# Kernel optimization log

Measured on AMD Instinct MI355X. Metric: run time of the kernel, lower is better.

The kernel has to match this reference:

```python
import jax, jax.numpy as jnp
import numpy as np

B, H, W = 2, 224, 224
E, NH, DH, DFF = 64, 4, 16, 2048


def _conv2d(x, w, b):
    # stride-1 3x3 conv, padding=1 == SAME
    y = jax.lax.conv_general_dilated(x, w, (1, 1), 'SAME',
                                     dimension_numbers=('NCHW', 'OIHW', 'NCHW'))
    return y + b[None, :, None, None]


def _layer_norm(x, g, b, eps=1e-5):
    mu = x.mean(-1, keepdims=True)
    xc = x - mu
    var = (xc * xc).mean(-1, keepdims=True)
    return g * xc * jax.lax.rsqrt(var + eps) + b


def setup_inputs() -> dict:
    key = jax.random.key(0)
    ks = jax.random.split(key, 16)
    rn = lambda k, shape, s=0.05: jax.random.normal(k, shape, dtype=jnp.float32) * s
    z = lambda n: jnp.zeros((n,), jnp.float32)
    return {
        'x': jax.random.normal(ks[0], (B, 3, H, W), dtype=jnp.float32),
        'enc_w1': rn(ks[1], (64, 3, 3, 3)), 'enc_b1': z(64),
        'enc_w2': rn(ks[2], (64, 64, 3, 3)), 'enc_b2': z(64),
        'in_proj_w': rn(ks[3], (3 * E, E)), 'in_proj_b': z(3 * E),
        'out_proj_w': rn(ks[4], (E, E)), 'out_proj_b': z(E),
        'ln1_g': jnp.ones((E,), jnp.float32), 'ln1_b': z(E),
        'ffn_w1': rn(ks[5], (DFF, E)), 'ffn_b1': z(DFF),
        'ffn_w2': rn(ks[6], (E, DFF)), 'ffn_b2': z(E),
        'ln2_g': jnp.ones((E,), jnp.float32), 'ln2_b': z(E),
        'sf_w1': rn(ks[7], (32, 64, 3, 3)), 'sf_b1': z(32),
        'sf_w2': rn(ks[8], (9, 32, 3, 3)), 'sf_b2': z(9),
        'dec_w1': rn(ks[9], (64, 1, 3, 3)), 'dec_b1': z(64),
        'dec_w2': rn(ks[10], (1, 64, 3, 3)), 'dec_b2': z(1),
    }


def _forward(x, enc_w1, enc_b1, enc_w2, enc_b2,
             in_proj_w, in_proj_b, out_proj_w, out_proj_b,
             ln1_g, ln1_b, ffn_w1, ffn_b1, ffn_w2, ffn_b2, ln2_g, ln2_b,
             sf_w1, sf_b1, sf_w2, sf_b2, dec_w1, dec_b1, dec_w2, dec_b2):
    # ---- encoder ----
    e = jax.nn.relu(_conv2d(x, enc_w1, enc_b1))
    e = jax.nn.relu(_conv2d(e, enc_w2, enc_b2))
    b, c, h, w = e.shape
    # torch TransformerEncoderLayer default batch_first=False: [B, HW, E] is (S=B, N=HW, E)
    t = e.reshape(b, c, h * w).transpose(0, 2, 1)  # [S=B, N=HW, E]
    qkv = t @ in_proj_w.T + in_proj_b
    q, k, v = jnp.split(qkv, 3, axis=-1)
    S, N = q.shape[0], q.shape[1]
    q = q.reshape(S, N, NH, DH)
    k = k.reshape(S, N, NH, DH)
    v = v.reshape(S, N, NH, DH)
    scores = jnp.einsum('snhd,tnhd->nhst', q, k) / np.float32(np.sqrt(DH))
    attn = jnp.einsum('nhst,tnhd->snhd', jax.nn.softmax(scores, axis=-1), v)
    attn = attn.reshape(S, N, E) @ out_proj_w.T + out_proj_b
    t = _layer_norm(t + attn, ln1_g, ln1_b)
    ff = jax.nn.relu(t @ ffn_w1.T + ffn_b1) @ ffn_w2.T + ffn_b2
    t = _layer_norm(t + ff, ln2_g, ln2_b)
    enc2 = t.transpose(0, 2, 1).reshape(b, c, h, w)
    # ---- spatially adaptive per-pixel 3x3 filter (KPN-style) ----
    f = _conv2d(_conv2d(enc2, sf_w1, sf_b1), sf_w2, sf_b2)
    filters = f.reshape(b, 3, 3, h, w)  # per-pixel 3x3 kernel
    s = x.sum(axis=1)  # accumulate over the 3 input channels -> [B,H,W]
    sp = jnp.pad(s, ((0, 0), (1, 1), (1, 1)))
    patches = jnp.stack([sp[:, u:u + h, v:v + w] for u in range(3) for v in range(3)],
                        axis=1).reshape(b, 3, 3, h, w)
    fused = (filters * patches).sum(axis=(1, 2))[:, None]  # [B,1,H,W]
    # ---- decoder ----
    d = jax.nn.relu(_conv2d(fused, dec_w1, dec_b1))
    return jax.nn.sigmoid(_conv2d(d, dec_w2, dec_b2))


def reference(x, enc_w1, enc_b1, enc_w2, enc_b2,
              in_proj_w, in_proj_b, out_proj_w, out_proj_b,
              ln1_g, ln1_b, ffn_w1, ffn_b1, ffn_w2, ffn_b2, ln2_g, ln2_b,
              sf_w1, sf_b1, sf_w2, sf_b2, dec_w1, dec_b1, dec_w2, dec_b2):
    return _forward(x, enc_w1, enc_b1, enc_w2, enc_b2,
                    in_proj_w, in_proj_b, out_proj_w, out_proj_b,
                    ln1_g, ln1_b, ffn_w1, ffn_b1, ffn_w2, ffn_b2, ln2_g, ln2_b,
                    sf_w1, sf_b1, sf_w2, sf_b2, dec_w1, dec_b1, dec_w2, dec_b2)
```

## Files before the change

kernel.cpp:

```cpp
#include <hip/hip_runtime.h>
#include <hip/hip_bf16.h>
#include <cstddef>

#define HW   50176
#define NPIX 100352
#define IW   224

typedef unsigned short ushort_t;
typedef __attribute__((ext_vector_type(8))) short bf16x8;
typedef __attribute__((ext_vector_type(8))) unsigned short ushort8;
typedef __attribute__((ext_vector_type(4))) float f32x4;
typedef __attribute__((ext_vector_type(2))) _Float16 f16x2;
typedef __attribute__((ext_vector_type(8))) _Float16 f16x8;

__device__ inline ushort_t f2bf(float f) {
    __hip_bfloat16 h = __float2bfloat16(f);
    return __builtin_bit_cast(ushort_t, h);
}
__device__ inline float bf2f(ushort_t u) {
    return __uint_as_float(((unsigned)u) << 16);
}
__device__ inline bf16x8 ldg8(const ushort_t* p) {
    return *reinterpret_cast<const bf16x8*>(p);
}
__device__ inline void b2f8(const ushort_t* p, float* f) {
    ushort8 v = *reinterpret_cast<const ushort8*>(p);
#pragma unroll
    for (int i = 0; i < 8; i++) f[i] = bf2f(v[i]);
}
__device__ inline f16x2 pk16(float a, float b) {
    return __builtin_bit_cast(f16x2, __builtin_amdgcn_cvt_pkrtz(a, b));
}

__device__ inline void dma16(const ushort_t* g, ushort_t* l) {
    __builtin_amdgcn_global_load_lds(
        (const __attribute__((address_space(1))) void*)g,
        (__attribute__((address_space(3))) void*)l, 16, 0, 0);
}

__device__ void conv1_body(int gid, const float* __restrict__ x,
                           const float* __restrict__ w,
                           const float* __restrict__ bias,
                           ushort_t* __restrict__ out)
{
    int b = gid >= HW;
    int p = gid - b * HW;
    int y = p / IW, xx = p - y * IW;

    float v[27];
#pragma unroll
    for (int ci = 0; ci < 3; ci++) {
        const float* ip = x + ((size_t)(b * 3 + ci)) * HW;
#pragma unroll
        for (int t = 0; t < 9; t++) {
            int dy = t / 3 - 1, dx = t % 3 - 1;
            int yy = y + dy, xc = xx + dx;
            float tv = 0.f;
            if ((unsigned)yy < (unsigned)IW && (unsigned)xc < (unsigned)IW)
                tv = ip[yy * IW + xc];
            v[ci * 9 + t] = tv;
        }
    }
#pragma unroll
    for (int g = 0; g < 8; g++) {
        ushort8 o8;
#pragma unroll
        for (int i = 0; i < 8; i++) {
            int co = g * 8 + i;
            float a = bias[co];
            const float* wp = w + co * 27;
#pragma unroll
            for (int k = 0; k < 27; k++) a = fmaf(v[k], wp[k], a);
            o8[i] = f2bf(fmaxf(a, 0.f));
        }
        *reinterpret_cast<ushort8*>(out + (size_t)gid * 64 + g * 8) = o8;
    }
}

__global__ __launch_bounds__(256) void prep_conv1_k(
    const float* __restrict__ x,     const float* __restrict__ enc_w1,
    const float* __restrict__ enc_b1, ushort_t* __restrict__ E1b,
    const float* __restrict__ in_w,  ushort_t* __restrict__ in_wb,
    const float* __restrict__ out_w, ushort_t* __restrict__ out_wb,
    const float* __restrict__ w1,    ushort_t* __restrict__ w1p,
    const float* __restrict__ w2,    _Float16* __restrict__ w2s,
    const float* __restrict__ ec2,   ushort_t* __restrict__ wc2p,
    const float* __restrict__ s1,    ushort_t* __restrict__ ws1p,
    const float* __restrict__ s2,    ushort_t* __restrict__ ws2)
{
    if (blockIdx.x < 392) {
        conv1_body(blockIdx.x * 256 + threadIdx.x, x, enc_w1, enc_b1, E1b);
        return;
    }
    int idx = (blockIdx.x - 392) * 256 + threadIdx.x;
    if (idx < 12288) { in_wb[idx] = f2bf(in_w[idx]); return; }
    idx -= 12288;
    if (idx < 4096)  { out_wb[idx] = f2bf(out_w[idx]); return; }
    idx -= 4096;
    if (idx < 131072){
        int j = idx >> 6, e = idx & 63;
        int c = j >> 6, jl = j & 63;
        w1p[(size_t)c * 6144 + jl * 72 + e] = f2bf(w1[idx]);
        return;
    }
    idx -= 131072;
    if (idx < 131072){
        int j    = idx & 7;
        int lane = (idx >> 3) & 63;
        int rest = idx >> 9;
        int nt   = rest & 3;
        int cp   = rest >> 2;
        int p    = cp & 1;
        int c    = cp >> 1;
        int quad = lane >> 4;
        int e2   = nt * 16 + (lane & 15);
        int hl   = (j < 4) ? (quad * 4 + j) : (16 + quad * 4 + (j - 4));
        int hidden = c * 64 + p * 32 + hl;
        w2s[idx] = (_Float16)w2[(size_t)e2 * 2048 + hidden];
        return;
    }
    idx -= 131072;
    if (idx < 36864) {
        int j    = idx & 7;
        int lane = (idx >> 3) & 63;
        int rest = idx >> 9;
        int ks   = rest & 1;
        int nt   = (rest >> 1) & 3;
        int t    = rest >> 3;
        int co   = nt * 16 + (lane & 15);
        int ci   = ks * 32 + (lane >> 4) * 8 + j;
        wc2p[idx] = f2bf(ec2[((size_t)co * 64 + ci) * 9 + t]);
        return;
    }
    idx -= 36864;
    if (idx < 18432) {
        int j    = idx & 7;
        int lane = (idx >> 3) & 63;
        int rest = idx >> 9;
        int ks   = rest & 1;
        int nt   = (rest >> 1) & 1;
        int t    = rest >> 2;
        int co   = nt * 16 + (lane & 15);
        int ci   = ks * 32 + (lane >> 4) * 8 + j;
        ws1p[idx] = f2bf(s1[((size_t)co * 64 + ci) * 9 + t]);
        return;
    }
    idx -= 18432;
    if (idx < 4608)  {
        int ci = idx % 32;
        int t  = (idx / 32) % 9;
        int co = idx / 288;
        ws2[idx] = (co < 9) ? f2bf(s2[((size_t)co * 32 + ci) * 9 + t]) : (ushort_t)0;
        return;
    }
}

__global__ __launch_bounds__(256, 2) void enc2xf_k(
    const ushort_t* __restrict__ E1b, const ushort_t* __restrict__ Wc2p,
    const float* __restrict__ enc_b2,
    const ushort_t* __restrict__ Wqkv, const float* __restrict__ Bqkv,
    const ushort_t* __restrict__ Wo, const float* __restrict__ Bo,
    const float* __restrict__ g, const float* __restrict__ be,
    ushort_t* __restrict__ T1b)
{
    __shared__ ushort_t Q[128 * 200];
    __shared__ ushort_t WT[9216];

    int tid = threadIdx.x, wave = tid >> 6, lane = tid & 63;
    int lm = lane & 15, quad = lane >> 4;
    int p0 = blockIdx.x * 64;

    {
        int lr0 = wave * 32;
        int m[2], py[2], px[2];
#pragma unroll
        for (int mt = 0; mt < 2; mt++) {
            int lr = lr0 + mt * 16 + lm;
            int gp = p0 + (lr & 63);
            m[mt] = (lr >> 6) * HW + gp;
            py[mt] = gp / IW;
            px[mt] = gp - py[mt] * IW;
        }

        f32x4 acc[2][4] = {};
        bf16x8 zz = {};
        bf16x8 af[9][2][2];

#pragma unroll
        for (int t = 0; t < 9; t++) {
            int dy = t / 3 - 1, dx = t % 3 - 1;
#pragma unroll
            for (int mt = 0; mt < 2; mt++) {
                bool ok = (unsigned)(py[mt] + dy) < (unsigned)IW &&
                          (unsigned)(px[mt] + dx) < (unsigned)IW;
                const ushort_t* ip = E1b + (size_t)(m[mt] + dy * IW + dx) * 64 + quad * 8;
#pragma unroll
                for (int ks = 0; ks < 2; ks++)
                    af[t][mt][ks] = ok ? ldg8(ip + ks * 32) : zz;
            }
        }

#pragma unroll
        for (int t = 0; t < 9; t++) {
#pragma unroll
            for (int nt = 0; nt < 4; nt++)
#pragma unroll
                for (int ks = 0; ks < 2; ks++) {
                    bf16x8 bfv = ldg8(Wc2p + (size_t)(t * 8 + nt * 2 + ks) * 512 + lane * 8);
#pragma unroll
                    for (int mt = 0; mt < 2; mt++)
                        acc[mt][nt] = __builtin_amdgcn_mfma_f32_16x16x32_bf16(
                            af[t][mt][ks], bfv, acc[mt][nt], 0, 0, 0);
                }
        }

#pragma unroll
        for (int nt = 0; nt < 4; nt++) {
            float bv = enc_b2[nt * 16 + lm];
#pragma unroll
            for (int mt = 0; mt < 2; mt++)
#pragma unroll
                for (int r = 0; r < 4; r++) {
                    int lr = lr0 + mt * 16 + quad * 4 + r;
                    WT[lr * 72 + nt * 16 + lm] =
                        f2bf(fmaxf(acc[mt][nt][r] + bv, 0.f));
                }
        }
    }

    bf16x8 wq[12][2];
#pragma unroll
    for (int nt = 0; nt < 12; nt++)
#pragma unroll
        for (int ks = 0; ks < 2; ks++)
            wq[nt][ks] = ldg8(Wqkv + (size_t)(nt * 16 + lm) * 64 + ks * 32 + quad * 8);

    __syncthreads();

#pragma unroll
    for (int mt = 0; mt < 2; mt++) {
        int lA = mt * 64 + wave * 16;
        bf16x8 a[2];
#pragma unroll
        for (int ks = 0; ks < 2; ks++)
            a[ks] = *reinterpret_cast<const bf16x8*>(
                &WT[(lA + lm) * 72 + ks * 32 + quad * 8]);
        f32x4 acc[12] = {};
#pragma unroll
        for (int nt = 0; nt < 12; nt++)
#pragma unroll
            for (int ks = 0; ks < 2; ks++)
                acc[nt] = __builtin_amdgcn_mfma_f32_16x16x32_bf16(
                    a[ks], wq[nt][ks], acc[nt], 0, 0, 0);
        int lrow = lA + quad * 4;
#pragma unroll
        for (int nt = 0; nt < 12; nt++) {
            float bb = Bqkv[nt * 16 + lm];
#pragma unroll
            for (int r = 0; r < 4; r++)
                Q[(lrow + r) * 200 + nt * 16 + lm] = f2bf(acc[nt][r] + bb);
        }
    }
    __syncthreads();

    {
        int px = tid >> 2, h = tid & 3;
        ushort_t* r0 = &Q[px * 200 + h * 16];
        ushort_t* r1 = &Q[(64 + px) * 200 + h * 16];

        float q0[16], k0[16], v0[16], q1[16], k1[16], v1[16];
        b2f8(r0,       q0); b2f8(r0 + 8,   q0 + 8);
        b2f8(r0 + 64,  k0); b2f8(r0 + 72,  k0 + 8);
        b2f8(r0 + 128, v0); b2f8(r0 + 136, v0 + 8);
        b2f8(r1,       q1); b2f8(r1 + 8,   q1 + 8);
        b2f8(r1 + 64,  k1); b2f8(r1 + 72,  k1 + 8);
        b2f8(r1 + 128, v1); b2f8(r1 + 136, v1 + 8);

        float s00 = 0, s01 = 0, s10 = 0, s11 = 0;
#pragma unroll
        for (int d = 0; d < 16; d++) {
            s00 += q0[d] * k0[d]; s01 += q0[d] * k1[d];
            s10 += q1[d] * k0[d]; s11 += q1[d] * k1[d];
        }
        s00 *= 0.25f; s01 *= 0.25f; s10 *= 0.25f; s11 *= 0.25f;

        float m0 = fmaxf(s00, s01);
        float e00 = __expf(s00 - m0), e01 = __expf(s01 - m0);
        float i0 = 1.f / (e00 + e01);
        float p00 = e00 * i0, p01 = e01 * i0;

        float m1 = fmaxf(s10, s11);
        float e10 = __expf(s10 - m1), e11 = __expf(s11 - m1);
        float i1 = 1.f / (e10 + e11);
        float p10 = e10 * i1, p11 = e11 * i1;

#pragma unroll
        for (int c = 0; c < 2; c++) {
            ushort8 a0v, a1v;
#pragma unroll
            for (int i = 0; i < 8; i++) {
                int d = c * 8 + i;
                a0v[i] = f2bf(p00 * v0[d] + p01 * v1[d]);
                a1v[i] = f2bf(p10 * v0[d] + p11 * v1[d]);
            }
            *reinterpret_cast<ushort8*>(r0 + c * 8) = a0v;
            *reinterpret_cast<ushort8*>(r1 + c * 8) = a1v;
        }
    }

    bf16x8 wo[4][2];
#pragma unroll
    for (int nt = 0; nt < 4; nt++)
#pragma unroll
        for (int ks = 0; ks < 2; ks++)
            wo[nt][ks] = ldg8(Wo + (size_t)(nt * 16 + lm) * 64 + ks * 32 + quad * 8);

    __syncthreads();

#pragma unroll
    for (int mt = 0; mt < 2; mt++) {
        int lA = mt * 64 + wave * 16;
        size_t gbase = (size_t)((mt == 0 ? p0 : HW + p0) + wave * 16);
        bf16x8 a[2];
#pragma unroll
        for (int ks = 0; ks < 2; ks++)
            a[ks] = *reinterpret_cast<const bf16x8*>(
                &Q[(lA + lm) * 200 + ks * 32 + quad * 8]);
        f32x4 acc[4] = {};
#pragma unroll
        for (int nt = 0; nt < 4; nt++)
#pragma unroll
            for (int ks = 0; ks < 2; ks++)
                acc[nt] = __builtin_amdgcn_mfma_f32_16x16x32_bf16(
                    a[ks], wo[nt][ks], acc[nt], 0, 0, 0);

        float bv[4], gv[4], bev[4];
#pragma unroll
        for (int nt = 0; nt < 4; nt++) {
            bv[nt]  = Bo[nt * 16 + lm];
            gv[nt]  = g[nt * 16 + lm];
            bev[nt] = be[nt * 16 + lm];
        }
#pragma unroll
        for (int r = 0; r < 4; r++) {
            int lr = lA + quad * 4 + r;
            size_t row = gbase + quad * 4 + r;
            float v[4]; float s = 0.f;
#pragma unroll
            for (int nt = 0; nt < 4; nt++) {
                v[nt] = acc[nt][r] + bv[nt] + bf2f(WT[lr * 72 + nt * 16 + lm]);
                s += v[nt];
            }
#pragma unroll
            for (int o = 8; o; o >>= 1) s += __shfl_xor(s, o, 64);
            float mu = s * 0.015625f;
            float q = 0.f;
#pragma unroll
            for (int nt = 0; nt < 4; nt++) { v[nt] -= mu; q += v[nt] * v[nt]; }
#pragma unroll
            for (int o = 8; o; o >>= 1) q += __shfl_xor(q, o, 64);
            float rstd = rsqrtf(q * 0.015625f + 1e-5f);
#pragma unroll
            for (int nt = 0; nt < 4; nt++)
                T1b[row * 64 + nt * 16 + lm] = f2bf(gv[nt] * v[nt] * rstd + bev[nt]);
        }
    }
}

__global__ __launch_bounds__(256, 2) void neconv2_k(
    const ushort_t* __restrict__ In, const ushort_t* __restrict__ Wp,
    const float* __restrict__ bias, ushort_t* __restrict__ Ob)
{
    int tid = threadIdx.x, wave = tid >> 6, lane = tid & 63;
    int lm = lane & 15, quad = lane >> 4;
    int m0 = blockIdx.x * 128 + wave * 32;

    int m[2], py[2], px[2];
#pragma unroll
    for (int mt = 0; mt < 2; mt++) {
        int mm = m0 + mt * 16 + lm;
        m[mt] = mm;
        int p = mm - (mm >= HW ? HW : 0);
        py[mt] = p / IW;
        px[mt] = p - py[mt] * IW;
    }

    f32x4 acc[2][2] = {};
    bf16x8 zz = {};
    bf16x8 af[9][2][2];

#pragma unroll
    for (int t = 0; t < 9; t++) {
        int dy = t / 3 - 1, dx = t % 3 - 1;
#pragma unroll
        for (int mt = 0; mt < 2; mt++) {
            bool ok = (unsigned)(py[mt] + dy) < (unsigned)IW &&
                      (unsigned)(px[mt] + dx) < (unsigned)IW;
            const ushort_t* ip = In + (size_t)(m[mt] + dy * IW + dx) * 64 + quad * 8;
#pragma unroll
            for (int ks = 0; ks < 2; ks++)
                af[t][mt][ks] = ok ? ldg8(ip + ks * 32) : zz;
        }
    }

#pragma unroll
    for (int t = 0; t < 9; t++) {
#pragma unroll
        for (int nt = 0; nt < 2; nt++)
#pragma unroll
            for (int ks = 0; ks < 2; ks++) {
                bf16x8 bfv = ldg8(Wp + (size_t)(t * 4 + nt * 2 + ks) * 512 + lane * 8);
#pragma unroll
                for (int mt = 0; mt < 2; mt++)
                    acc[mt][nt] = __builtin_amdgcn_mfma_f32_16x16x32_bf16(
                        af[t][mt][ks], bfv, acc[mt][nt], 0, 0, 0);
            }
    }

#pragma unroll
    for (int nt = 0; nt < 2; nt++) {
        int col = nt * 16 + lm;
        float bv = bias[col];
#pragma unroll
        for (int mt = 0; mt < 2; mt++)
#pragma unroll
            for (int r = 0; r < 4; r++) {
                int row = m0 + mt * 16 + quad * 4 + r;
                Ob[(size_t)row * 32 + col] = f2bf(acc[mt][nt][r] + bv);
            }
    }
}

__global__ __launch_bounds__(512) void ffn9_k(
    const ushort_t* __restrict__ T1b,
    const ushort_t* __restrict__ W1p, const float* __restrict__ B1,
    const _Float16* __restrict__ W2s, const float* __restrict__ B2,
    const float* __restrict__ g, const float* __restrict__ be,
    ushort_t* __restrict__ OutTb)
{
    __shared__ ushort_t W1lds[3][6144];
    __shared__ ushort_t W2lds[3][4096];
    __shared__ float    B1l[2048];

    int tid = threadIdx.x, wave = tid >> 6, lane = tid & 63;
    int lm = lane & 15, quad = lane >> 4;
    int rowbase = blockIdx.x * 256 + wave * 32;

    *reinterpret_cast<float4*>(&B1l[tid * 4]) =
        *reinterpret_cast<const float4*>(B1 + tid * 4);

    bf16x8 Bt[2][2];
#pragma unroll
    for (int mt = 0; mt < 2; mt++)
#pragma unroll
        for (int ks = 0; ks < 2; ks++)
            Bt[mt][ks] = ldg8(T1b + (size_t)(rowbase + mt * 16 + lm) * 64 + ks * 32 + quad * 8);

    __syncthreads();

    auto dma_chunk = [&](int c, int pb) {
        const ushort_t* g1 = W1p + (size_t)c * 6144;
        const ushort_t* g2 = (const ushort_t*)(W2s + (size_t)c * 4096);
#pragma unroll
        for (int i = 0; i < 3; i++) {
            int idx = i * 8 + wave;
            if (idx < 12)
                dma16(g1 + idx * 512 + lane * 8, &W1lds[pb][idx * 512]);
            else if (idx < 20)
                dma16(g2 + (idx - 12) * 512 + lane * 8,
                      &W2lds[pb][(idx - 12) * 512]);
        }
    };

    dma_chunk(0, 0);
    dma_chunk(1, 1);

    f32x4 acc[2][4] = {};

    for (int c = 0; c < 32; c++) {
        int pb = c % 3;

        if (c < 31) {
            if (wave < 4) asm volatile("s_waitcnt vmcnt(3)" ::: "memory");
            else          asm volatile("s_waitcnt vmcnt(2)" ::: "memory");
        } else {
            asm volatile("s_waitcnt vmcnt(0)" ::: "memory");
        }
        __builtin_amdgcn_s_barrier();
        asm volatile("" ::: "memory");

        if (c + 2 < 32) dma_chunk(c + 2, (c + 2) % 3);

        const ushort_t* w1l = &W1lds[pb][0];
        const ushort_t* w2l = &W2lds[pb][0];

#pragma unroll
        for (int p = 0; p < 2; p++) {
            bf16x8 w1r[2][2];
            f16x8  w2r[4];
            float4 b1r[2];
#pragma unroll
            for (int s = 0; s < 2; s++) {
                int ul = p * 2 + s;
#pragma unroll
                for (int ks = 0; ks < 2; ks++)
                    w1r[s][ks] = *reinterpret_cast<const bf16x8*>(
                        &w1l[(ul * 16 + lm) * 72 + ks * 32 + quad * 8]);
                b1r[s] = *reinterpret_cast<const float4*>(
                    &B1l[(c * 4 + ul) * 16 + quad * 4]);
            }
#pragma unroll
            for (int nt = 0; nt < 4; nt++)
                w2r[nt] = *reinterpret_cast<const f16x8*>(
                    &w2l[((p * 4 + nt) * 64 + lane) * 8]);

            f32x4 h[2][2];
#pragma unroll
            for (int s = 0; s < 2; s++) {
                f32x4 binit = {b1r[s].x, b1r[s].y, b1r[s].z, b1r[s].w};
#pragma unroll
                for (int mt = 0; mt < 2; mt++) h[s][mt] = binit;
            }

            __builtin_amdgcn_s_setprio(1);
#pragma unroll
            for (int s = 0; s < 2; s++)
#pragma unroll
                for (int ks = 0; ks < 2; ks++)
#pragma unroll
                    for (int mt = 0; mt < 2; mt++)
                        h[s][mt] = __builtin_amdgcn_mfma_f32_16x16x32_bf16(
                            w1r[s][ks], Bt[mt][ks], h[s][mt], 0, 0, 0);

            f16x8 aH[2];
#pragma unroll
            for (int mt = 0; mt < 2; mt++) {
                f16x2 t0 = pk16(fmaxf(h[0][mt][0], 0.f), fmaxf(h[0][mt][1], 0.f));
                f16x2 t1 = pk16(fmaxf(h[0][mt][2], 0.f), fmaxf(h[0][mt][3], 0.f));
                f16x2 t2 = pk16(fmaxf(h[1][mt][0], 0.f), fmaxf(h[1][mt][1], 0.f));
                f16x2 t3 = pk16(fmaxf(h[1][mt][2], 0.f), fmaxf(h[1][mt][3], 0.f));
                f16x8 a;
                a[0] = t0[0]; a[1] = t0[1]; a[2] = t1[0]; a[3] = t1[1];
                a[4] = t2[0]; a[5] = t2[1]; a[6] = t3[0]; a[7] = t3[1];
                aH[mt] = a;
            }

#pragma unroll
            for (int nt = 0; nt < 4; nt++)
#pragma unroll
                for (int mt = 0; mt < 2; mt++)
                    acc[mt][nt] = __builtin_amdgcn_mfma_f32_16x16x32_f16(
                        aH[mt], w2r[nt], acc[mt][nt], 0, 0, 0);
            __builtin_amdgcn_s_setprio(0);
        }
    }

    float b2v[4], gv[4], bev[4];
#pragma unroll
    for (int nt = 0; nt < 4; nt++) {
        b2v[nt] = B2[nt * 16 + lm];
        gv[nt]  = g[nt * 16 + lm];
        bev[nt] = be[nt * 16 + lm];
    }
#pragma unroll
    for (int mt = 0; mt < 2; mt++)
#pragma unroll
        for (int r = 0; r < 4; r++) {
            int row = rowbase + mt * 16 + quad * 4 + r;
            float v[4]; float s = 0.f;
#pragma unroll
            for (int nt = 0; nt < 4; nt++) {
                v[nt] = acc[mt][nt][r] + b2v[nt] +
                        bf2f(T1b[(size_t)row * 64 + nt * 16 + lm]);
                s += v[nt];
            }
#pragma unroll
            for (int o = 8; o; o >>= 1) s += __shfl_xor(s, o, 64);
            float mu = s * 0.015625f;
            float q = 0.f;
#pragma unroll
            for (int nt = 0; nt < 4; nt++) { v[nt] -= mu; q += v[nt] * v[nt]; }
#pragma unroll
            for (int o = 8; o; o >>= 1) q += __shfl_xor(q, o, 64);
            float rstd = rsqrtf(q * 0.015625f + 1e-5f);
#pragma unroll
            for (int nt = 0; nt < 4; nt++)
                OutTb[(size_t)row * 64 + nt * 16 + lm] =
                    f2bf(gv[nt] * v[nt] * rstd + bev[nt]);
        }
}

__global__ __launch_bounds__(256) void sf2kpn_k(
    const ushort_t* __restrict__ In,
    const ushort_t* __restrict__ Wsw,
    const float* __restrict__ bias,
    const float* __restrict__ x,
    float* __restrict__ fused)
{
    __shared__ float Fl[128 * 12];
    int tid = threadIdx.x, wave = tid >> 6, lane = tid & 63;
    int lm = lane & 15, quad = lane >> 4;
    int m0 = blockIdx.x * 128 + wave * 32;

    int m[2], py[2], px[2];
#pragma unroll
    for (int mt = 0; mt < 2; mt++) {
        int mm = m0 + mt * 16 + lm;
        m[mt] = mm;
        int p = mm - (mm >= HW ? HW : 0);
        py[mt] = p / IW;
        px[mt] = p - py[mt] * IW;
    }

    f32x4 acc[2] = {};
    bf16x8 zz = {};
    bf16x8 af[9][2];
    bf16x8 wv[9];

#pragma unroll
    for (int t = 0; t < 9; t++) {
        int dy = t / 3 - 1, dx = t % 3 - 1;
#pragma unroll
        for (int mt = 0; mt < 2; mt++) {
            bool ok = (unsigned)(py[mt] + dy) < (unsigned)IW &&
                      (unsigned)(px[mt] + dx) < (unsigned)IW;
            af[t][mt] = ok ? ldg8(In + (size_t)(m[mt] + dy * IW + dx) * 32 + quad * 8) : zz;
        }
    }
#pragma unroll
    for (int t = 0; t < 9; t++)
        wv[t] = ldg8(Wsw + ((size_t)lm * 9 + t) * 32 + quad * 8);

#pragma unroll
    for (int t = 0; t < 9; t++)
#pragma unroll
        for (int mt = 0; mt < 2; mt++)
            acc[mt] = __builtin_amdgcn_mfma_f32_16x16x32_bf16(af[t][mt], wv[t], acc[mt], 0, 0, 0);

    if (lm < 9) {
        float bv = bias[lm];
#pragma unroll
        for (int mt = 0; mt < 2; mt++)
#pragma unroll
            for (int r = 0; r < 4; r++) {
                int lrow = wave * 32 + mt * 16 + quad * 4 + r;
                Fl[lrow * 12 + lm] = acc[mt][r] + bv;
            }
    }
    __syncthreads();

    if (tid < 128) {
        int gid = blockIdx.x * 128 + tid;
        int b = gid >= HW;
        int p = gid - b * HW;
        int y = p / IW, xx = p - y * IW;
        const float* fp = &Fl[tid * 12];
        const float* xp = x + (size_t)b * 3 * HW;
        float a = 0.f;
#pragma unroll
        for (int u = 0; u < 3; u++) {
            int yy = y + u - 1;
            if ((unsigned)yy >= (unsigned)IW) continue;
#pragma unroll
            for (int v = 0; v < 3; v++) {
                int xc = xx + v - 1;
                if ((unsigned)xc >= (unsigned)IW) continue;
                int o = yy * IW + xc;
                float s = xp[o] + xp[HW + o] + xp[2 * HW + o];
                a += fp[u * 3 + v] * s;
            }
        }
        fused[gid] = a;
    }
}

__global__ __launch_bounds__(256) void dec_tile_k(
    const float* __restrict__ fused,
    const float* __restrict__ w1, const float* __restrict__ b1,
    const float* __restrict__ w2, const float* __restrict__ b2,
    float* __restrict__ out)
{
    __shared__ float    Fs[400];
    __shared__ _Float16 Hl[324 * 72];

    int tid = threadIdx.x;
    int b   = blockIdx.x / 196;
    int rem = blockIdx.x - b * 196;
    int ty0 = (rem / 14) * 16;
    int tx0 = (rem % 14) * 16;
    const float* fp = fused + (size_t)b * HW;

    for (int k = tid; k < 400; k += 256) {
        int fy = k / 20, fx = k - fy * 20;
        int gy = ty0 + fy - 2, gx = tx0 + fx - 2;
        float t = 0.f;
        if ((unsigned)gy < (unsigned)IW && (unsigned)gx < (unsigned)IW)
            t = fp[gy * IW + gx];
        Fs[k] = t;
    }
    __syncthreads();

    for (int ph = tid; ph < 324; ph += 256) {
        int hy = ph / 18, hx = ph - hy * 18;
        int gy = ty0 + hy - 1, gx = tx0 + hx - 1;
        _Float16* op = &Hl[ph * 72];
        if ((unsigned)gy >= (unsigned)IW || (unsigned)gx >= (unsigned)IW) {
            f16x8 z = {};
#pragma unroll
            for (int g = 0; g < 8; g++)
                *reinterpret_cast<f16x8*>(op + g * 8) = z;
        } else {
            float F[9];
#pragma unroll
            for (int s = 0; s < 9; s++)
                F[s] = Fs[(hy + s / 3) * 20 + (hx + s % 3)];
#pragma unroll
            for (int g = 0; g < 8; g++) {
                f16x8 o;
#pragma unroll
                for (int i = 0; i < 8; i++) {
                    int c = g * 8 + i;
                    float h = b1[c];
                    const float* wp = w1 + c * 9;
#pragma unroll
                    for (int s = 0; s < 9; s++) h = fmaf(F[s], wp[s], h);
                    o[i] = (_Float16)fmaxf(h, 0.f);
                }
                *reinterpret_cast<f16x8*>(op + g * 8) = o;
            }
        }
    }
    __syncthreads();

    {
        int ty = tid >> 4, tx = tid & 15;
        int gy = ty0 + ty, gx = tx0 + tx;
        float acc = b2[0];
#pragma unroll
        for (int n = 0; n < 9; n++) {
            int dy = n / 3 - 1, dx = n % 3 - 1;
            int yy = gy + dy, xc = gx + dx;
            if ((unsigned)yy >= (unsigned)IW || (unsigned)xc >= (unsigned)IW) continue;
            const _Float16* hp = &Hl[((ty + 1 + dy) * 18 + (tx + 1 + dx)) * 72];
#pragma unroll
            for (int g = 0; g < 8; g++) {
                f16x8 hv = *reinterpret_cast<const f16x8*>(hp + g * 8);
#pragma unroll
                for (int i = 0; i < 8; i++)
                    acc = fmaf((float)hv[i], w2[(g * 8 + i) * 9 + n], acc);
            }
        }
        out[(size_t)b * HW + gy * IW + gx] = 1.f / (1.f + __expf(-acc));
    }
}

extern "C" void kernel_launch(void* const* d_in, const int* in_sizes, int n_in,
                              void* d_out, int out_size, void* d_ws, size_t ws_size,
                              hipStream_t stream)
{
    const float* x      = (const float*)d_in[0];
    const float* enc_w1 = (const float*)d_in[1];
    const float* enc_b1 = (const float*)d_in[2];
    const float* enc_w2 = (const float*)d_in[3];
    const float* enc_b2 = (const float*)d_in[4];
    const float* in_w   = (const float*)d_in[5];
    const float* in_b   = (const float*)d_in[6];
    const float* out_w  = (const float*)d_in[7];
    const float* out_b  = (const float*)d_in[8];
    const float* ln1_g  = (const float*)d_in[9];
    const float* ln1_b  = (const float*)d_in[10];
    const float* ffn_w1 = (const float*)d_in[11];
    const float* ffn_b1 = (const float*)d_in[12];
    const float* ffn_w2 = (const float*)d_in[13];
    const float* ffn_b2 = (const float*)d_in[14];
    const float* ln2_g  = (const float*)d_in[15];
    const float* ln2_b  = (const float*)d_in[16];
    const float* sf_w1  = (const float*)d_in[17];
    const float* sf_b1  = (const float*)d_in[18];
    const float* sf_w2  = (const float*)d_in[19];
    const float* sf_b2  = (const float*)d_in[20];
    const float* dec_w1 = (const float*)d_in[21];
    const float* dec_b1 = (const float*)d_in[22];
    const float* dec_w2 = (const float*)d_in[23];
    const float* dec_b2 = (const float*)d_in[24];

    float* ws = (float*)d_ws;
    const size_t SZ = (size_t)NPIX * 64;

    ushort_t* E1b  = (ushort_t*)(ws + 5 * SZ);
    ushort_t* Tb   = (ushort_t*)(ws + 11 * SZ / 2);
    ushort_t* wu   = (ushort_t*)(ws + 6 * SZ);
    ushort_t* in_wb  = wu;
    ushort_t* out_wb = wu + 12288;
    ushort_t* w1p    = wu + 16384;
    _Float16* w2s    = (_Float16*)(wu + 212992);
    ushort_t* wc2p   = wu + 344064;
    ushort_t* ws1p   = wu + 385536;
    ushort_t* ws2    = wu + 408576;
    float*    base3 = ws + 3 * SZ;
    ushort_t* s1b   = (ushort_t*)base3;
    float*    fused = base3 + SZ / 2;

    prep_conv1_k<<<1714, 256, 0, stream>>>(
        x, enc_w1, enc_b1, E1b,
        in_w, in_wb, out_w, out_wb, ffn_w1, w1p,
        ffn_w2, w2s, enc_w2, wc2p, sf_w1, ws1p, sf_w2, ws2);

    enc2xf_k<<<784, 256, 0, stream>>>(E1b, wc2p, enc_b2,
                                      in_wb, in_b, out_wb, out_b,
                                      ln1_g, ln1_b, Tb);
    ffn9_k<<<392, 512, 0, stream>>>(Tb, w1p, ffn_b1, w2s, ffn_b2, ln2_g, ln2_b, E1b);
    neconv2_k<<<784, 256, 0, stream>>>(E1b, ws1p, sf_b1, s1b);
    sf2kpn_k<<<784, 256, 0, stream>>>(s1b, ws2, sf_b2, x, fused);
    dec_tile_k<<<392, 256, 0, stream>>>(fused, dec_w1, dec_b1, dec_w2, dec_b2,
                                        (float*)d_out);
}
```

Measured before the change: 297.2 us.

## Halve enc2xf tile to 32 pixels per block and raise occupancy

The fused encoder-conv2 + attention kernel now handles 32 pixels (64 rows across both batch items) per block instead of 64. Each wave computes one M-tile instead of two, and the QKV weights are loaded inside the MFMA loop instead of being kept in registers. Shared memory is roughly halved and launch bounds go from 2 to 4 blocks per CU, which should raise occupancy and latency hiding. In exchange, twice as many blocks are launched, so weights are reloaded more often per pixel, and half the threads sit idle during the attention step.

```diff
diff --git a/kernel.cpp b/kernel.cpp
--- a/kernel.cpp
+++ b/kernel.cpp
@@ -155,7 +155,7 @@
     }
 }
 
-__global__ __launch_bounds__(256, 2) void enc2xf_k(
+__global__ __launch_bounds__(256, 4) void enc2xf_k(
     const ushort_t* __restrict__ E1b, const ushort_t* __restrict__ Wc2p,
     const float* __restrict__ enc_b2,
     const ushort_t* __restrict__ Wqkv, const float* __restrict__ Bqkv,
@@ -163,41 +163,33 @@
     const float* __restrict__ g, const float* __restrict__ be,
     ushort_t* __restrict__ T1b)
 {
-    __shared__ ushort_t Q[128 * 200];
-    __shared__ ushort_t WT[9216];
+    __shared__ ushort_t Q[64 * 200];
+    __shared__ ushort_t WT[64 * 72];
 
     int tid = threadIdx.x, wave = tid >> 6, lane = tid & 63;
     int lm = lane & 15, quad = lane >> 4;
-    int p0 = blockIdx.x * 64;
+    int p0 = blockIdx.x * 32;
 
     {
-        int lr0 = wave * 32;
-        int m[2], py[2], px[2];
-#pragma unroll
-        for (int mt = 0; mt < 2; mt++) {
-            int lr = lr0 + mt * 16 + lm;
-            int gp = p0 + (lr & 63);
-            m[mt] = (lr >> 6) * HW + gp;
-            py[mt] = gp / IW;
-            px[mt] = gp - py[mt] * IW;
-        }
-
-        f32x4 acc[2][4] = {};
+        int lr0 = wave * 16;
+        int lr  = lr0 + lm;
+        int gp  = p0 + (lr & 31);
+        int mm  = (lr >> 5) * HW + gp;
+        int py  = gp / IW, px = gp - py * IW;
+
+        f32x4 acc[4] = {};
         bf16x8 zz = {};
-        bf16x8 af[9][2][2];
+        bf16x8 af[9][2];
 
 #pragma unroll
         for (int t = 0; t < 9; t++) {
             int dy = t / 3 - 1, dx = t % 3 - 1;
-#pragma unroll
-            for (int mt = 0; mt < 2; mt++) {
-                bool ok = (unsigned)(py[mt] + dy) < (unsigned)IW &&
-                          (unsigned)(px[mt] + dx) < (unsigned)IW;
-                const ushort_t* ip = E1b + (size_t)(m[mt] + dy * IW + dx) * 64 + quad * 8;
-#pragma unroll
-                for (int ks = 0; ks < 2; ks++)
-                    af[t][mt][ks] = ok ? ldg8(ip + ks * 32) : zz;
-            }
+            bool ok = (unsigned)(py + dy) < (unsigned)IW &&
+                      (unsigned)(px + dx) < (unsigned)IW;
+            const ushort_t* ip = E1b + (size_t)(mm + dy * IW + dx) * 64 + quad * 8;
+#pragma unroll
+            for (int ks = 0; ks < 2; ks++)
+                af[t][ks] = ok ? ldg8(ip + ks * 32) : zz;
         }
 
 #pragma unroll
@@ -207,10 +199,8 @@
 #pragma unroll
                 for (int ks = 0; ks < 2; ks++) {
                     bf16x8 bfv = ldg8(Wc2p + (size_t)(t * 8 + nt * 2 + ks) * 512 + lane * 8);
-#pragma unroll
-                    for (int mt = 0; mt < 2; mt++)
-                        acc[mt][nt] = __builtin_amdgcn_mfma_f32_16x16x32_bf16(
-                            af[t][mt][ks], bfv, acc[mt][nt], 0, 0, 0);
+                    acc[nt] = __builtin_amdgcn_mfma_f32_16x16x32_bf16(
+                        af[t][ks], bfv, acc[nt], 0, 0, 0);
                 }
         }
 
@@ -218,28 +208,17 @@
         for (int nt = 0; nt < 4; nt++) {
             float bv = enc_b2[nt * 16 + lm];
 #pragma unroll
-            for (int mt = 0; mt < 2; mt++)
-#pragma unroll
-                for (int r = 0; r < 4; r++) {
-                    int lr = lr0 + mt * 16 + quad * 4 + r;
-                    WT[lr * 72 + nt * 16 + lm] =
-                        f2bf(fmaxf(acc[mt][nt][r] + bv, 0.f));
-                }
-        }
-    }
-
-    bf16x8 wq[12][2];
-#pragma unroll
-    for (int nt = 0; nt < 12; nt++)
-#pragma unroll
-        for (int ks = 0; ks < 2; ks++)
-            wq[nt][ks] = ldg8(Wqkv + (size_t)(nt * 16 + lm) * 64 + ks * 32 + quad * 8);
-
+            for (int r = 0; r < 4; r++) {
+                int wr = lr0 + quad * 4 + r;
+                WT[wr * 72 + nt * 16 + lm] =
+                    f2bf(fmaxf(acc[nt][r] + bv, 0.f));
+            }
+        }
+    }
     __syncthreads();
 
-#pragma unroll
-    for (int mt = 0; mt < 2; mt++) {
-        int lA = mt * 64 + wave * 16;
+    {
+        int lA = wave * 16;
         bf16x8 a[2];
 #pragma unroll
         for (int ks = 0; ks < 2; ks++)
@@ -249,9 +228,11 @@
 #pragma unroll
         for (int nt = 0; nt < 12; nt++)
 #pragma unroll
-            for (int ks = 0; ks < 2; ks++)
+            for (int ks = 0; ks < 2; ks++) {
+                bf16x8 b = ldg8(Wqkv + (size_t)(nt * 16 + lm) * 64 + ks * 32 + quad * 8);
                 acc[nt] = __builtin_amdgcn_mfma_f32_16x16x32_bf16(
-                    a[ks], wq[nt][ks], acc[nt], 0, 0, 0);
+                    a[ks], b, acc[nt], 0, 0, 0);
+            }
         int lrow = lA + quad * 4;
 #pragma unroll
         for (int nt = 0; nt < 12; nt++) {
@@ -263,10 +244,10 @@
     }
     __syncthreads();
 
-    {
+    if (tid < 128) {
         int px = tid >> 2, h = tid & 3;
         ushort_t* r0 = &Q[px * 200 + h * 16];
-        ushort_t* r1 = &Q[(64 + px) * 200 + h * 16];
+        ushort_t* r1 = &Q[(32 + px) * 200 + h * 16];
 
         float q0[16], k0[16], v0[16], q1[16], k1[16], v1[16];
         b2f8(r0,       q0); b2f8(r0 + 8,   q0 + 8);
@@ -317,10 +298,9 @@
 
     __syncthreads();
 
-#pragma unroll
-    for (int mt = 0; mt < 2; mt++) {
-        int lA = mt * 64 + wave * 16;
-        size_t gbase = (size_t)((mt == 0 ? p0 : HW + p0) + wave * 16);
+    {
+        int lA = wave * 16;
+        size_t gbase = (size_t)((lA >> 5) * HW + p0 + (lA & 31));
         bf16x8 a[2];
 #pragma unroll
         for (int ks = 0; ks < 2; ks++)
@@ -806,9 +786,9 @@
         in_w, in_wb, out_w, out_wb, ffn_w1, w1p,
         ffn_w2, w2s, enc_w2, wc2p, sf_w1, ws1p, sf_w2, ws2);
 
-    enc2xf_k<<<784, 256, 0, stream>>>(E1b, wc2p, enc_b2,
-                                      in_wb, in_b, out_wb, out_b,
-                                      ln1_g, ln1_b, Tb);
+    enc2xf_k<<<1568, 256, 0, stream>>>(E1b, wc2p, enc_b2,
+                                       in_wb, in_b, out_wb, out_b,
+                                       ln1_g, ln1_b, Tb);
     ffn9_k<<<392, 512, 0, stream>>>(Tb, w1p, ffn_b1, w2s, ffn_b2, ln2_g, ln2_b, E1b);
     neconv2_k<<<784, 256, 0, stream>>>(E1b, ws1p, sf_b1, s1b);
     sf2kpn_k<<<784, 256, 0, stream>>>(s1b, ws2, sf_b2, x, fused);
```

Measured after the change: 302.3 us. Within noise of the previous version (+1.7%).
